# Performance work log

Hardware: AMD Instinct MI355X
Metric: run time of the kernel (lower is better)

## Reference

```python
import jax, jax.numpy as jnp
import numpy as np

GROUPS = 32
EPS = 1e-5


def group_norm(x, scale, bias):
    b, c, h, w = x.shape
    xg = x.reshape(b, GROUPS, c // GROUPS, h, w)
    mean = jnp.mean(xg, axis=(2, 3, 4), keepdims=True)
    var = jnp.var(xg, axis=(2, 3, 4), keepdims=True)
    xn = (xg - mean) * jax.lax.rsqrt(var + EPS)
    xn = xn.reshape(b, c, h, w)
    return xn * scale[None, :, None, None] + bias[None, :, None, None]


def conv1x1(x, w, b):
    # x: [b,c,h,w], w: [out,in] -> [b,out,h,w]
    return jnp.einsum('bchw,oc->bohw', x, w) + b[None, :, None, None]


def setup_inputs() -> dict:
    key = jax.random.key(0)
    ks = jax.random.split(key, 8)
    B, C, H, W = 4, 512, 64, 64
    s = 1.0 / np.sqrt(C)
    return {
        'x': jax.random.normal(ks[0], (B, C, H, W), jnp.float32),
        'norm_scale': jnp.ones((C,), jnp.float32),
        'norm_bias': jnp.zeros((C,), jnp.float32),
        'wq': jax.random.normal(ks[1], (C, C), jnp.float32) * s,
        'bq': jnp.zeros((C,), jnp.float32),
        'wk': jax.random.normal(ks[2], (C, C), jnp.float32) * s,
        'bk': jnp.zeros((C,), jnp.float32),
        'wv': jax.random.normal(ks[3], (C, C), jnp.float32) * s,
        'bv': jnp.zeros((C,), jnp.float32),
        'wo': jax.random.normal(ks[4], (C, C), jnp.float32) * s,
        'bo': jnp.zeros((C,), jnp.float32),
    }


def reference(x, norm_scale, norm_bias, wq, bq, wk, bk, wv, bv, wo, bo):
    b, c, h, w = x.shape
    hn = group_norm(x, norm_scale, norm_bias)
    q = conv1x1(hn, wq, bq)  # [b,c,h,w]
    k = conv1x1(hn, wk, bk)
    v = conv1x1(hn, wv, bv)
    n = h * w
    q = q.reshape(b, c, n).transpose(0, 2, 1)  # [b,n,c]
    k = k.reshape(b, c, n)                     # [b,c,n]
    v = v.reshape(b, c, n).transpose(0, 2, 1)  # [b,n,c]
    scale = jnp.asarray(c, x.dtype) ** -0.5
    attn = jax.nn.softmax(jnp.einsum('bic,bcj->bij', q, k) * scale, axis=-1)
    out = jnp.einsum('bij,bjc->bic', attn, v)  # [b,n,c]
    out = out.transpose(0, 2, 1).reshape(b, c, h, w)
    return x + conv1x1(out, wo, bo)
```

## Files before the change

kernel.cpp:

```cpp
#include <hip/hip_runtime.h>
#include <math.h>

#define B_ 4
#define C_ 512
#define N_ 4096
#define NG 32

typedef __attribute__((ext_vector_type(4))) float f32x4;
typedef __attribute__((ext_vector_type(8))) short bf16x8;
typedef __attribute__((ext_vector_type(8))) unsigned short u16x8;
typedef __attribute__((ext_vector_type(4))) unsigned short u16x4;

__device__ __forceinline__ unsigned short f2bf(float f){
  unsigned u = __float_as_uint(f);
  return (unsigned short)((u + 0x7fffu + ((u >> 16) & 1u)) >> 16);
}
__device__ __forceinline__ float bf2f(unsigned short h){
  return __uint_as_float(((unsigned)h) << 16);
}

__global__ __launch_bounds__(256) void gn_stats_k(const float* __restrict__ x, float* __restrict__ stats){
  int bg = blockIdx.x;
  const float4* xp = (const float4*)(x + (size_t)bg * 65536);
  float s = 0.f, ss = 0.f;
  for (int i = threadIdx.x; i < 16384; i += 256){
    float4 v = xp[i];
    s  += v.x + v.y + v.z + v.w;
    ss += v.x*v.x + v.y*v.y + v.z*v.z + v.w*v.w;
  }
  __shared__ float ls[256], lq[256];
  ls[threadIdx.x] = s; lq[threadIdx.x] = ss;
  __syncthreads();
  for (int o = 128; o > 0; o >>= 1){
    if (threadIdx.x < o){ ls[threadIdx.x] += ls[threadIdx.x+o]; lq[threadIdx.x] += lq[threadIdx.x+o]; }
    __syncthreads();
  }
  if (threadIdx.x == 0){
    float mean = ls[0] * (1.f/65536.f);
    float var  = lq[0] * (1.f/65536.f) - mean*mean;
    stats[bg*2+0] = mean;
    stats[bg*2+1] = rsqrtf(var + 1e-5f);
  }
}

__global__ __launch_bounds__(256) void gn_apply_k(const float* __restrict__ x, const float* __restrict__ stats,
    const float* __restrict__ gam, const float* __restrict__ bet, unsigned short* __restrict__ hn){
  __shared__ unsigned short tile[C_][33];
  int b = blockIdx.y, n0 = blockIdx.x * 32;
  const float* xb = x + (size_t)b * C_ * N_;
  for (int i = threadIdx.x; i < 4096; i += 256){
    int c = i >> 3, j4 = (i & 7) * 4;
    float4 v = *(const float4*)(xb + (size_t)c * N_ + n0 + j4);
    int g = c >> 4;
    float mean = stats[(b*NG+g)*2], rstd = stats[(b*NG+g)*2+1];
    float sc = gam[c] * rstd;
    float bi = bet[c] - mean * sc;
    tile[c][j4+0] = f2bf(v.x*sc+bi);
    tile[c][j4+1] = f2bf(v.y*sc+bi);
    tile[c][j4+2] = f2bf(v.z*sc+bi);
    tile[c][j4+3] = f2bf(v.w*sc+bi);
  }
  __syncthreads();
  for (int i = threadIdx.x; i < 2048; i += 256){
    int cc = (i & 63) * 8, j = i >> 6;
    u16x8 o;
    #pragma unroll
    for (int t = 0; t < 8; t++) o[t] = tile[cc+t][j];
    *(u16x8*)(hn + ((size_t)b*N_ + n0 + j) * C_ + cc) = o;
  }
}

__global__ __launch_bounds__(256) void prep_w_k(const float* __restrict__ wq, const float* __restrict__ wk,
    const float* __restrict__ wv, const float* __restrict__ wo,
    unsigned short* __restrict__ wqkv, unsigned short* __restrict__ wob, float scl){
  int i = blockIdx.x * 256 + threadIdx.x;
  int mat = i >> 16, idx = i & 65535;
  const float* src = (mat==0) ? wq : (mat==1) ? wk : (mat==2) ? wv : wo;
  float s = (mat==0) ? scl : 1.f;
  float4 v = ((const float4*)src)[idx];
  u16x4 o; o[0]=f2bf(v.x*s); o[1]=f2bf(v.y*s); o[2]=f2bf(v.z*s); o[3]=f2bf(v.w*s);
  if (mat < 3) ((u16x4*)wqkv)[mat*65536 + idx] = o;
  else         ((u16x4*)wob)[idx] = o;
}

__global__ __launch_bounds__(256) void prep_b_k(const float* __restrict__ bq, const float* __restrict__ bk,
    const float* __restrict__ bv, float* __restrict__ bqkv, float scl){
  int i = blockIdx.x * 256 + threadIdx.x;
  if (i < 512) bqkv[i] = bq[i] * scl;
  else if (i < 1024) bqkv[i] = bk[i-512];
  else if (i < 1536) bqkv[i] = bv[i-1024];
}

template<int BIAS_MODE , bool OUT_BF16, bool RESID>
__global__ __launch_bounds__(256) void gemm_bt_k(
    const unsigned short* __restrict__ A, const unsigned short* __restrict__ Bt,
    void* __restrict__ Cv, const float* __restrict__ bias, const float* __restrict__ resid,
    int Ncols, int K, int lda, int ldb,
    long long sA, long long sB, long long sC, long long sR, float scale)
{
  const int tid = threadIdx.x;
  const int bz = blockIdx.z;
  A  += (size_t)bz * sA;
  Bt += (size_t)bz * sB;

  const int nwg = gridDim.x * gridDim.y;
  const int wg  = blockIdx.y * gridDim.x + blockIdx.x;
  const int swz = (wg & 7) * (nwg >> 3) + (wg >> 3);
  const int bx = swz % gridDim.x, by = swz / gridDim.x;

  const int tn = bx * 128, tm = by * 128;
  __shared__ unsigned short lA[2][128*32];
  __shared__ unsigned short lB[2][128*32];
  const int wave = tid >> 6, lane = tid & 63;
  const int wm = (wave >> 1) * 64, wn = (wave & 1) * 64;
  f32x4 acc[4][4] = {};

  const unsigned short* Abase = A + (size_t)tm * lda;
  const unsigned short* Bbase = Bt + (size_t)tn * ldb;

  const int srow = tid >> 2, pch = tid & 3;
  const int sch  = pch ^ ((srow >> 1) & 3);
  const size_t aoff0 = (size_t)srow      * lda + sch*8;
  const size_t aoff1 = (size_t)(srow+64) * lda + sch*8;
  const size_t boff0 = (size_t)srow      * ldb + sch*8;
  const size_t boff1 = (size_t)(srow+64) * ldb + sch*8;
  const int ldst0 = srow*32      + pch*8;
  const int ldst1 = (srow+64)*32 + pch*8;

  auto issue = [&](int buf, int k0){
    __builtin_amdgcn_global_load_lds((const __attribute__((address_space(1))) unsigned int*)(Abase + aoff0 + k0),
        (__attribute__((address_space(3))) unsigned int*)(&lA[buf][ldst0]), 16, 0, 0);
    __builtin_amdgcn_global_load_lds((const __attribute__((address_space(1))) unsigned int*)(Bbase + boff0 + k0),
        (__attribute__((address_space(3))) unsigned int*)(&lB[buf][ldst0]), 16, 0, 0);
    __builtin_amdgcn_global_load_lds((const __attribute__((address_space(1))) unsigned int*)(Abase + aoff1 + k0),
        (__attribute__((address_space(3))) unsigned int*)(&lA[buf][ldst1]), 16, 0, 0);
    __builtin_amdgcn_global_load_lds((const __attribute__((address_space(1))) unsigned int*)(Bbase + boff1 + k0),
        (__attribute__((address_space(3))) unsigned int*)(&lB[buf][ldst1]), 16, 0, 0);
  };

  issue(0, 0);
  __syncthreads();
  const int T = K >> 5;
  for (int t = 0; t < T; t++){
    const int cur = t & 1;
    if (t + 1 < T) issue(cur ^ 1, (t + 1) << 5);

    bf16x8 af[4], bfb[4];
    const int lr = lane & 15, q = lane >> 4;
    #pragma unroll
    for (int i = 0; i < 4; i++){
      int row = wm + i*16 + lr;
      af[i]  = *(const bf16x8*)&lA[cur][row*32 + ((q ^ ((row >> 1) & 3)) * 8)];
    }
    #pragma unroll
    for (int j = 0; j < 4; j++){
      int row = wn + j*16 + lr;
      bfb[j] = *(const bf16x8*)&lB[cur][row*32 + ((q ^ ((row >> 1) & 3)) * 8)];
    }
    #pragma unroll
    for (int i = 0; i < 4; i++)
      #pragma unroll
      for (int j = 0; j < 4; j++)
        acc[i][j] = __builtin_amdgcn_mfma_f32_16x16x32_bf16(af[i], bfb[j], acc[i][j], 0, 0, 0);

    __syncthreads();
  }

  const int rr = (lane >> 4) * 4, cl = lane & 15;
  #pragma unroll
  for (int i = 0; i < 4; i++){
    #pragma unroll
    for (int j = 0; j < 4; j++){
      int col = tn + wn + j*16 + cl;
      float cb = (BIAS_MODE == 1) ? bias[col] : 0.f;
      #pragma unroll
      for (int r = 0; r < 4; r++){
        int row = tm + wm + i*16 + rr + r;
        float v = acc[i][j][r];
        if (BIAS_MODE == 1) v += cb;
        if (BIAS_MODE == 2) v += bias[row];
        v *= scale;
        size_t idx = (size_t)bz * sC + (size_t)row * Ncols + col;
        if (RESID) v += resid[(size_t)bz * sR + (size_t)row * Ncols + col];
        if (OUT_BF16) ((unsigned short*)Cv)[idx] = f2bf(v);
        else          ((float*)Cv)[idx] = v;
      }
    }
  }
}

__global__ __launch_bounds__(256) void transpose_v_k(const unsigned short* __restrict__ QKV, unsigned short* __restrict__ Vt){
  __shared__ unsigned short t[64][72];
  int b = blockIdx.z, c0 = blockIdx.x * 64, n0 = blockIdx.y * 64;
  int tid = threadIdx.x;
  for (int i = tid; i < 512; i += 256){
    int n = i >> 3, cc = (i & 7) * 8;
    u16x8 v = *(const u16x8*)&QKV[((size_t)b*N_ + n0 + n)*1536 + 1024 + c0 + cc];
    #pragma unroll
    for (int j = 0; j < 8; j++) t[cc+j][n] = v[j];
  }
  __syncthreads();
  for (int i = tid; i < 512; i += 256){
    int c = i >> 3, nn = (i & 7) * 8;
    u16x8 o;
    #pragma unroll
    for (int j = 0; j < 8; j++) o[j] = t[c][nn+j];
    *(u16x8*)&Vt[((size_t)b*C_ + c0 + c)*N_ + n0 + nn] = o;
  }
}

__global__ __launch_bounds__(256) void softmax_k(unsigned short* __restrict__ SP){
  size_t row = blockIdx.x;
  u16x8* sp = (u16x8*)(SP + row * 4096);
  const int t = threadIdx.x;
  u16x8 h0 = sp[t], h1 = sp[t + 256];
  float v[16];
  #pragma unroll
  for (int j = 0; j < 8; j++){ v[j] = bf2f(h0[j]); v[8+j] = bf2f(h1[j]); }
  float m = -3.0e38f;
  #pragma unroll
  for (int j = 0; j < 16; j++) m = fmaxf(m, v[j]);
  #pragma unroll
  for (int o = 32; o > 0; o >>= 1) m = fmaxf(m, __shfl_xor(m, o));
  __shared__ float red[4], red2[4];
  if ((t & 63) == 0) red[t >> 6] = m;
  __syncthreads();
  m = fmaxf(fmaxf(red[0], red[1]), fmaxf(red[2], red[3]));
  float s = 0.f;
  #pragma unroll
  for (int j = 0; j < 16; j++){ float e = __expf(v[j] - m); v[j] = e; s += e; }
  #pragma unroll
  for (int o = 32; o > 0; o >>= 1) s += __shfl_xor(s, o);
  if ((t & 63) == 0) red2[t >> 6] = s;
  __syncthreads();
  s = red2[0] + red2[1] + red2[2] + red2[3];
  float inv = 1.0f / s;
  u16x8 o0, o1;
  #pragma unroll
  for (int j = 0; j < 8; j++){ o0[j] = f2bf(v[j] * inv); o1[j] = f2bf(v[8+j] * inv); }
  sp[t] = o0; sp[t + 256] = o1;
}

extern "C" void kernel_launch(void* const* d_in, const int* in_sizes, int n_in,
                              void* d_out, int out_size, void* d_ws, size_t ws_size,
                              hipStream_t stream)
{
  (void)in_sizes; (void)n_in; (void)out_size;
  const float* x   = (const float*)d_in[0];
  const float* gam = (const float*)d_in[1];
  const float* bet = (const float*)d_in[2];
  const float* wq  = (const float*)d_in[3];
  const float* bq  = (const float*)d_in[4];
  const float* wk  = (const float*)d_in[5];
  const float* bk  = (const float*)d_in[6];
  const float* wv  = (const float*)d_in[7];
  const float* bv  = (const float*)d_in[8];
  const float* wo  = (const float*)d_in[9];
  const float* bo  = (const float*)d_in[10];

  char* ws = (char*)d_ws;
  size_t off = 0;
  auto alloc = [&](size_t bytes)->void*{ void* p = ws + off; off += (bytes + 255) & ~(size_t)255; return p; };
  unsigned short* hn   = (unsigned short*)alloc((size_t)B_*N_*C_*2);
  unsigned short* QKV  = (unsigned short*)alloc((size_t)B_*N_*1536*2);
  unsigned short* Vt   = (unsigned short*)alloc((size_t)B_*C_*N_*2);
  unsigned short* O    = (unsigned short*)alloc((size_t)B_*N_*C_*2);
  unsigned short* wqkv = (unsigned short*)alloc((size_t)3*C_*C_*2);
  unsigned short* wob  = (unsigned short*)alloc((size_t)C_*C_*2);
  float* bqkv          = (float*)alloc(1536*4);
  float* stats         = (float*)alloc((size_t)B_*NG*2*4);

  size_t base = off;
  long long avail = (long long)ws_size - (long long)base;
  long long per_row = (long long)N_*2;
  long long rows_ll = avail > 0 ? avail / per_row : 0;
  int rows = (int)(rows_ll > 16384 ? 16384 : rows_ll);
  rows = (rows / 128) * 128;
  if (rows < 128) rows = 128;
  unsigned short* S = (unsigned short*)(ws + base);

  const float scl = 0.044194173824159216f;
  const long long NC  = (long long)N_ * C_;
  const long long CN  = (long long)C_ * N_;
  const long long NN  = (long long)N_ * N_;
  const long long NC3 = (long long)N_ * 1536;

  prep_w_k<<<dim3(1024), 256, 0, stream>>>(wq, wk, wv, wo, wqkv, wob, scl);
  prep_b_k<<<dim3(6),    256, 0, stream>>>(bq, bk, bv, bqkv, scl);

  gn_stats_k<<<dim3(B_*NG), 256, 0, stream>>>(x, stats);
  gn_apply_k<<<dim3(N_/32, B_), 256, 0, stream>>>(x, stats, gam, bet, hn);

  gemm_bt_k<1,true,false><<<dim3(1536/128, B_*N_/128, 1), 256, 0, stream>>>(
      hn, wqkv, QKV, bqkv, nullptr, 1536, C_, C_, C_, 0,0,0,0, 1.f);

  transpose_v_k<<<dim3(C_/64, N_/64, B_), 256, 0, stream>>>(QKV, Vt);

  if (rows >= B_*N_){
    gemm_bt_k<0,true,false><<<dim3(N_/128, N_/128, B_), 256, 0, stream>>>(
        QKV, QKV + 512, S, nullptr, nullptr, N_, C_, 1536, 1536, NC3, NC3, NN, 0, 1.f);
    softmax_k<<<dim3(B_*N_), 256, 0, stream>>>(S);
    gemm_bt_k<0,true,false><<<dim3(C_/128, N_/128, B_), 256, 0, stream>>>(
        S, Vt, O, nullptr, nullptr, C_, N_, N_, N_, NN, CN, NC, 0, 1.f);
  } else {
    int CH = rows > N_ ? N_ : rows;
    for (int b = 0; b < B_; b++){
      for (int r0 = 0; r0 < N_; r0 += CH){
        int ch = (N_ - r0) < CH ? (N_ - r0) : CH;
        gemm_bt_k<0,true,false><<<dim3(N_/128, ch/128, 1), 256, 0, stream>>>(
            QKV + ((size_t)b*N_ + r0)*1536, QKV + (size_t)b*N_*1536 + 512, S, nullptr, nullptr,
            N_, C_, 1536, 1536, 0,0,0,0, 1.f);
        softmax_k<<<dim3(ch), 256, 0, stream>>>(S);
        gemm_bt_k<0,true,false><<<dim3(C_/128, ch/128, 1), 256, 0, stream>>>(
            S, Vt + (size_t)b*C_*N_, O + ((size_t)b*N_ + r0)*C_, nullptr, nullptr,
            C_, N_, N_, N_, 0,0,0,0, 1.f);
      }
    }
  }

  gemm_bt_k<2,false,true><<<dim3(N_/128, C_/128, B_), 256, 0, stream>>>(
      wob, O, (float*)d_out, bo, x, N_, C_, C_, C_, 0, NC, CN, CN, 1.f);
}
```

Baseline: 340.4 us.

## Switch GEMM to 32x32x16 MFMA and process attention in two batch halves

The GEMM kernel now uses the 32x32x16 bf16 MFMA with 2x2 f32x16 accumulators per wave in place of the 4x4 grid of 16x16x32 MFMAs. LDS fragment loads and the epilogue row mapping are rewritten to match the new register layout. The aim is fewer MFMA issues and fewer LDS reads per tile. Separately, the attention score/softmax/PV path now runs in two passes of two batches each, which halves the score-matrix footprint so it stays smaller in cache, at the cost of extra launches.

Result: slower. 404.7 us (+18.9%).

```diff
diff --git a/kernel.cpp b/kernel.cpp
--- a/kernel.cpp
+++ b/kernel.cpp
@@ -7,6 +7,7 @@
 #define NG 32
 
 typedef __attribute__((ext_vector_type(4))) float f32x4;
+typedef __attribute__((ext_vector_type(16))) float f32x16;
 typedef __attribute__((ext_vector_type(8))) short bf16x8;
 typedef __attribute__((ext_vector_type(8))) unsigned short u16x8;
 typedef __attribute__((ext_vector_type(4))) unsigned short u16x4;
@@ -113,7 +114,7 @@
   __shared__ unsigned short lB[2][128*32];
   const int wave = tid >> 6, lane = tid & 63;
   const int wm = (wave >> 1) * 64, wn = (wave & 1) * 64;
-  f32x4 acc[4][4] = {};
+  f32x16 acc[2][2] = {};
 
   const unsigned short* Abase = A + (size_t)tm * lda;
   const unsigned short* Bbase = Bt + (size_t)tn * ldb;
@@ -145,37 +146,43 @@
     const int cur = t & 1;
     if (t + 1 < T) issue(cur ^ 1, (t + 1) << 5);
 
-    bf16x8 af[4], bfb[4];
-    const int lr = lane & 15, q = lane >> 4;
-    #pragma unroll
-    for (int i = 0; i < 4; i++){
-      int row = wm + i*16 + lr;
-      af[i]  = *(const bf16x8*)&lA[cur][row*32 + ((q ^ ((row >> 1) & 3)) * 8)];
-    }
-    #pragma unroll
-    for (int j = 0; j < 4; j++){
-      int row = wn + j*16 + lr;
-      bfb[j] = *(const bf16x8*)&lB[cur][row*32 + ((q ^ ((row >> 1) & 3)) * 8)];
-    }
-    #pragma unroll
-    for (int i = 0; i < 4; i++)
+    bf16x8 af[2][2], bfb[2][2];
+    const int lr = lane & 31, hi = lane >> 5;
+    #pragma unroll
+    for (int i = 0; i < 2; i++){
+      int row = wm + i*32 + lr;
+      int xm = (row >> 1) & 3;
+      af[i][0] = *(const bf16x8*)&lA[cur][row*32 + ((hi     ^ xm) * 8)];
+      af[i][1] = *(const bf16x8*)&lA[cur][row*32 + (((2|hi) ^ xm) * 8)];
+    }
+    #pragma unroll
+    for (int j = 0; j < 2; j++){
+      int row = wn + j*32 + lr;
+      int xm = (row >> 1) & 3;
+      bfb[j][0] = *(const bf16x8*)&lB[cur][row*32 + ((hi     ^ xm) * 8)];
+      bfb[j][1] = *(const bf16x8*)&lB[cur][row*32 + (((2|hi) ^ xm) * 8)];
+    }
+    #pragma unroll
+    for (int ks = 0; ks < 2; ks++)
       #pragma unroll
-      for (int j = 0; j < 4; j++)
-        acc[i][j] = __builtin_amdgcn_mfma_f32_16x16x32_bf16(af[i], bfb[j], acc[i][j], 0, 0, 0);
+      for (int i = 0; i < 2; i++)
+        #pragma unroll
+        for (int j = 0; j < 2; j++)
+          acc[i][j] = __builtin_amdgcn_mfma_f32_32x32x16_bf16(af[i][ks], bfb[j][ks], acc[i][j], 0, 0, 0);
 
     __syncthreads();
   }
 
-  const int rr = (lane >> 4) * 4, cl = lane & 15;
-  #pragma unroll
-  for (int i = 0; i < 4; i++){
-    #pragma unroll
-    for (int j = 0; j < 4; j++){
-      int col = tn + wn + j*16 + cl;
+  const int cl = lane & 31, rhi = (lane >> 5) * 4;
+  #pragma unroll
+  for (int i = 0; i < 2; i++){
+    #pragma unroll
+    for (int j = 0; j < 2; j++){
+      int col = tn + wn + j*32 + cl;
       float cb = (BIAS_MODE == 1) ? bias[col] : 0.f;
       #pragma unroll
-      for (int r = 0; r < 4; r++){
-        int row = tm + wm + i*16 + rr + r;
+      for (int r = 0; r < 16; r++){
+        int row = tm + wm + i*32 + (r & 3) + 8*(r >> 2) + rhi;
         float v = acc[i][j][r];
         if (BIAS_MODE == 1) v += cb;
         if (BIAS_MODE == 2) v += bias[row];
@@ -296,12 +303,16 @@
 
   transpose_v_k<<<dim3(C_/64, N_/64, B_), 256, 0, stream>>>(QKV, Vt);
 
-  if (rows >= B_*N_){
-    gemm_bt_k<0,true,false><<<dim3(N_/128, N_/128, B_), 256, 0, stream>>>(
-        QKV, QKV + 512, S, nullptr, nullptr, N_, C_, 1536, 1536, NC3, NC3, NN, 0, 1.f);
-    softmax_k<<<dim3(B_*N_), 256, 0, stream>>>(S);
-    gemm_bt_k<0,true,false><<<dim3(C_/128, N_/128, B_), 256, 0, stream>>>(
-        S, Vt, O, nullptr, nullptr, C_, N_, N_, N_, NN, CN, NC, 0, 1.f);
+  if (rows >= 2*N_){
+    for (int p = 0; p < 2; p++){
+      gemm_bt_k<0,true,false><<<dim3(N_/128, N_/128, 2), 256, 0, stream>>>(
+          QKV + (size_t)p*2*NC3, QKV + (size_t)p*2*NC3 + 512, S, nullptr, nullptr,
+          N_, C_, 1536, 1536, NC3, NC3, NN, 0, 1.f);
+      softmax_k<<<dim3(2*N_), 256, 0, stream>>>(S);
+      gemm_bt_k<0,true,false><<<dim3(C_/128, N_/128, 2), 256, 0, stream>>>(
+          S, Vt + (size_t)p*2*CN, O + (size_t)p*2*NC, nullptr, nullptr,
+          C_, N_, N_, N_, NN, CN, NC, 0, 1.f);
+    }
   } else {
     int CH = rows > N_ ? N_ : rows;
     for (int b = 0; b < B_; b++){
```
